# Kernel optimization log

Hardware: AMD Instinct MI355X
Metric: run time of the kernel (lower is better)

## Reference

```python
import jax, jax.numpy as jnp
import numpy as np

B, H, N, D = 2, 16, 2048, 128

def setup_inputs() -> dict:
    key = jax.random.key(0)
    kq, kk, kv = jax.random.split(key, 3)
    q = jax.random.normal(kq, (B, H, N, D), dtype=jnp.float32)
    k = jax.random.normal(kk, (B, H, N, D), dtype=jnp.float32)
    v = jax.random.normal(kv, (B, H, N, D), dtype=jnp.float32)
    return {"q": q, "k": k, "v": v}

def reference(q, k, v):
    # scale = 1/sqrt(d) computed at forward time (scale=None in __init__)
    d = q.shape[-1]
    scale = 1.0 / jnp.sqrt(jnp.asarray(d, dtype=q.dtype))
    # scores: (B, H, N, N)
    scores = jnp.einsum('bhnd,bhmd->bhnm', q, k) * scale
    probs = jax.nn.softmax(scores, axis=-1)
    return jnp.einsum('bhnm,bhmd->bhnd', probs, v)
```

## Files before the change

kernel.cpp:

```cpp
#include <hip/hip_runtime.h>
#include <hip/hip_fp16.h>

#define BH   32
#define SEQ  2048
#define DIM  128
#define CK   32
#define NCH  (SEQ / CK)

typedef _Float16 half8   __attribute__((ext_vector_type(8)));
typedef __fp16   fp16x2  __attribute__((ext_vector_type(2)));
typedef _Float16 half2v  __attribute__((ext_vector_type(2)));
typedef float    floatx4 __attribute__((ext_vector_type(4)));

__device__ inline half2v pk2(float a, float b) {
    fp16x2 t = __builtin_amdgcn_cvt_pkrtz(a, b);
    return *(half2v*)&t;
}
__device__ inline half8 pk8(float4 a, float4 b) {
    half2v l0 = pk2(a.x, a.y), l1 = pk2(a.z, a.w);
    half2v l2 = pk2(b.x, b.y), l3 = pk2(b.z, b.w);
    half8 h;
    h[0] = l0[0]; h[1] = l0[1]; h[2] = l1[0]; h[3] = l1[1];
    h[4] = l2[0]; h[5] = l2[1]; h[6] = l3[0]; h[7] = l3[1];
    return h;
}

__device__ inline void ld16(const void* g, void* l) {
    __builtin_amdgcn_global_load_lds(
        (__attribute__((address_space(1))) void*)(uintptr_t)g,
        (__attribute__((address_space(3))) void*)(uintptr_t)l, 16, 0, 0);
}

#define SYNC_VM8 do {                                          \
    asm volatile("s_waitcnt vmcnt(8)" ::: "memory");           \
    __builtin_amdgcn_s_barrier();                              \
    asm volatile("" ::: "memory");                             \
} while (0)

__global__ void prep_kernel(const float* __restrict__ k, const float* __restrict__ v,
                            _Float16* __restrict__ kh, _Float16* __restrict__ vt) {
    const float SC = 0.08838834764831845f * 1.4426950408889634f;
    __shared__ __align__(16) _Float16 t[32][136];
    const int bh = blockIdx.x >> 6;
    const int kc = blockIdx.x & 63;
    const int tid = threadIdx.x;
    const size_t base = ((size_t)bh * SEQ + kc * CK) * DIM;

    const float4* kf4 = (const float4*)(k + base);
    const float4* vf4 = (const float4*)(v + base);
    half8* kh8 = (half8*)(kh + base);

    #pragma unroll
    for (int i = 0; i < 2; i++) {
        int f8 = i * 256 + tid;
        float4 a = kf4[2 * f8], b = kf4[2 * f8 + 1];
        a.x *= SC; a.y *= SC; a.z *= SC; a.w *= SC;
        b.x *= SC; b.y *= SC; b.z *= SC; b.w *= SC;
        kh8[f8] = pk8(a, b);
        int row = f8 >> 4, c8 = f8 & 15;
        *((half8*)&t[row][c8 * 8]) = pk8(vf4[2 * f8], vf4[2 * f8 + 1]);
    }
    __syncthreads();
    _Float16* vout = vt + ((size_t)bh * NCH + kc) * (DIM * CK);
    #pragma unroll
    for (int i = 0; i < 2; i++) {
        int g = i * 256 + tid;
        int d = g >> 2, kg = g & 3;
        half8 h;
        #pragma unroll
        for (int j = 0; j < 8; j++) h[j] = t[kg * 8 + j][d];
        *((half8*)(vout + d * CK + kg * 8)) = h;
    }
}

__global__ __launch_bounds__(256, 2) void attn_kernel(
        const float* __restrict__ q, const _Float16* __restrict__ kh,
        const _Float16* __restrict__ vt, float* __restrict__ out) {
    __shared__ __align__(16) _Float16 Kbuf[2][CK * DIM];

    const int lid = blockIdx.x + (blockIdx.y << 4);
    const int xcd = lid & 7;
    const int idx = lid >> 3;
    const int bh  = (xcd << 2) + (idx >> 4);
    const int qt  = idx & 15;

    const int tid  = threadIdx.x;
    const int w    = tid >> 6;
    const int lane = tid & 63;
    const int l15  = lane & 15;
    const int quad = lane >> 4;

    half8 qf[2][4];
    #pragma unroll
    for (int s = 0; s < 2; s++) {
        const float* qb = q + ((size_t)bh * SEQ + qt * 128 + w * 32 + s * 16 + l15) * DIM;
        #pragma unroll
        for (int c = 0; c < 4; c++) {
            float4 a = *((const float4*)(qb + c * 32 + quad * 8));
            float4 b = *((const float4*)(qb + c * 32 + quad * 8 + 4));
            qf[s][c] = pk8(a, b);
        }
    }

    half8 ones;
    #pragma unroll
    for (int j = 0; j < 8; j++) ones[j] = (_Float16)1.0f;

    floatx4 zf = {0.f, 0.f, 0.f, 0.f};
    floatx4 O[2][8];
    #pragma unroll
    for (int s = 0; s < 2; s++)
        #pragma unroll
        for (int i = 0; i < 8; i++) O[s][i] = zf;
    floatx4 Osum[2] = {zf, zf};

    const _Float16* kb = kh + (size_t)bh * SEQ * DIM;
    const _Float16* vb = vt + (size_t)bh * SEQ * DIM;

    const int s0 = w * 128 + lane;
    const int s1 = s0 + 64;
    const int rho0 = s0 >> 4, Pos0 = s0 & 15;
    const int rho1 = s1 >> 4, Pos1 = s1 & 15;
    const int g0 = (Pos0 - 3 * rho0) & 15;
    const int g1 = (Pos1 - 3 * rho1) & 15;
    const int key0 = (((rho0 >> 2) & 3) << 3) + ((rho0 >> 4) << 2) + (rho0 & 3);
    const int key1 = (((rho1 >> 2) & 3) << 3) + ((rho1 >> 4) << 2) + (rho1 & 3);
    const _Float16* kgp0 = kb + key0 * DIM + g0 * 8;
    const _Float16* kgp1 = kb + key1 * DIM + g1 * 8;

    auto dma = [&](int kc, int bk_) {
        size_t off = (size_t)kc * (CK * DIM);
        ld16(kgp0 + off, &Kbuf[bk_][(w * 2 + 0) * 512]);
        ld16(kgp1 + off, &Kbuf[bk_][(w * 2 + 1) * 512]);
    };

    const _Float16* vlp = vb + l15 * CK + quad * 8;
    half8 vfr[8];
    auto vload = [&](int kc) {
        const _Float16* p = vlp + (size_t)kc * (CK * DIM);
        #pragma unroll
        for (int dt = 0; dt < 8; dt++)
            vfr[dt] = *((const half8*)(p + dt * 512));
    };

    half8 pf0, pf1;
    #pragma unroll
    for (int j = 0; j < 8; j++) { pf0[j] = (_Float16)0.0f; pf1[j] = (_Float16)0.0f; }

    dma(0, 0);
    vload(0);

    #pragma unroll 2
    for (int kc = 0; kc < NCH; kc++) {
        SYNC_VM8;
        if (kc + 1 < NCH) dma(kc + 1, (kc + 1) & 1);

        const _Float16* Kc = Kbuf[kc & 1];

        floatx4 S[2][2];
        #pragma unroll
        for (int s = 0; s < 2; s++) { S[s][0] = zf; S[s][1] = zf; }
        __builtin_amdgcn_s_setprio(1);
        #pragma unroll
        for (int c = 0; c < 4; c++) {
            #pragma unroll
            for (int j = 0; j < 2; j++) {
                int rho = j * 16 + l15;
                int Pos = (c * 4 + quad + 3 * rho) & 15;
                half8 ka = *((const half8*)&Kc[rho * DIM + Pos * 8]);
                S[0][j] = __builtin_amdgcn_mfma_f32_16x16x32_f16(ka, qf[0][c], S[0][j], 0, 0, 0);
                S[1][j] = __builtin_amdgcn_mfma_f32_16x16x32_f16(ka, qf[1][c], S[1][j], 0, 0, 0);
            }
        }
        __builtin_amdgcn_s_setprio(0);

        half8 pn0, pn1;
        {
            float4 a, b;
            a.x = __builtin_amdgcn_exp2f(S[0][0][0]);
            a.y = __builtin_amdgcn_exp2f(S[0][0][1]);
            a.z = __builtin_amdgcn_exp2f(S[0][0][2]);
            a.w = __builtin_amdgcn_exp2f(S[0][0][3]);
            b.x = __builtin_amdgcn_exp2f(S[0][1][0]);
            b.y = __builtin_amdgcn_exp2f(S[0][1][1]);
            b.z = __builtin_amdgcn_exp2f(S[0][1][2]);
            b.w = __builtin_amdgcn_exp2f(S[0][1][3]);
            pn0 = pk8(a, b);
            a.x = __builtin_amdgcn_exp2f(S[1][0][0]);
            a.y = __builtin_amdgcn_exp2f(S[1][0][1]);
            a.z = __builtin_amdgcn_exp2f(S[1][0][2]);
            a.w = __builtin_amdgcn_exp2f(S[1][0][3]);
            b.x = __builtin_amdgcn_exp2f(S[1][1][0]);
            b.y = __builtin_amdgcn_exp2f(S[1][1][1]);
            b.z = __builtin_amdgcn_exp2f(S[1][1][2]);
            b.w = __builtin_amdgcn_exp2f(S[1][1][3]);
            pn1 = pk8(a, b);
        }

        __builtin_amdgcn_s_setprio(1);
        Osum[0] = __builtin_amdgcn_mfma_f32_16x16x32_f16(pf0, ones, Osum[0], 0, 0, 0);
        Osum[1] = __builtin_amdgcn_mfma_f32_16x16x32_f16(pf1, ones, Osum[1], 0, 0, 0);
        #pragma unroll
        for (int dt = 0; dt < 8; dt++) {
            O[0][dt] = __builtin_amdgcn_mfma_f32_16x16x32_f16(pf0, vfr[dt], O[0][dt], 0, 0, 0);
            O[1][dt] = __builtin_amdgcn_mfma_f32_16x16x32_f16(pf1, vfr[dt], O[1][dt], 0, 0, 0);
        }
        __builtin_amdgcn_s_setprio(0);

        vload(kc);

        pf0 = pn0; pf1 = pn1;
    }

    {
        __builtin_amdgcn_s_setprio(1);
        Osum[0] = __builtin_amdgcn_mfma_f32_16x16x32_f16(pf0, ones, Osum[0], 0, 0, 0);
        Osum[1] = __builtin_amdgcn_mfma_f32_16x16x32_f16(pf1, ones, Osum[1], 0, 0, 0);
        #pragma unroll
        for (int dt = 0; dt < 8; dt++) {
            O[0][dt] = __builtin_amdgcn_mfma_f32_16x16x32_f16(pf0, vfr[dt], O[0][dt], 0, 0, 0);
            O[1][dt] = __builtin_amdgcn_mfma_f32_16x16x32_f16(pf1, vfr[dt], O[1][dt], 0, 0, 0);
        }
        __builtin_amdgcn_s_setprio(0);
    }

    #pragma unroll
    for (int s = 0; s < 2; s++) {
        float* ob = out + ((size_t)bh * SEQ + qt * 128 + w * 32 + s * 16) * DIM;
        #pragma unroll
        for (int r = 0; r < 4; r++) {
            float rinv = 1.0f / Osum[s][r];
            #pragma unroll
            for (int dt = 0; dt < 8; dt++) {
                ob[(size_t)(quad * 4 + r) * DIM + dt * 16 + l15] = O[s][dt][r] * rinv;
            }
        }
    }
}

extern "C" void kernel_launch(void* const* d_in, const int* in_sizes, int n_in,
                              void* d_out, int out_size, void* d_ws, size_t ws_size,
                              hipStream_t stream) {
    const float* q = (const float*)d_in[0];
    const float* k = (const float*)d_in[1];
    const float* v = (const float*)d_in[2];
    float* out = (float*)d_out;

    const size_t elems = (size_t)BH * SEQ * DIM;
    _Float16* kh = (_Float16*)d_ws;
    _Float16* vtp = kh + elems;

    prep_kernel<<<BH * NCH, 256, 0, stream>>>(k, v, kh, vtp);
    attn_kernel<<<dim3(SEQ / 128, BH), 256, 0, stream>>>(q, kh, vtp, out);
}
```

Measured before the change: 207.5 us.

## Split key range across two warp groups and stage V through LDS

Doubles the block to 512 threads. Two groups of four waves each process half of the key chunks for the same 128 query rows, and their partial O and row sums are merged through shared memory at the end. V tiles are now DMA'd into a triple-buffered LDS region alongside K instead of being loaded from global memory into registers, and the wait changes to vmcnt(0). This raises parallelism per query tile and shortens the serial key loop. In exchange it uses more LDS and adds a reduction step, and the launch-bounds change may limit registers.

```diff
diff --git a/kernel.cpp b/kernel.cpp
--- a/kernel.cpp
+++ b/kernel.cpp
@@ -6,6 +6,8 @@
 #define DIM  128
 #define CK   32
 #define NCH  (SEQ / CK)
+#define NSTEP (NCH / 2)
+#define CSZ  (CK * DIM)
 
 typedef _Float16 half8   __attribute__((ext_vector_type(8)));
 typedef __fp16   fp16x2  __attribute__((ext_vector_type(2)));
@@ -31,8 +33,8 @@
         (__attribute__((address_space(3))) void*)(uintptr_t)l, 16, 0, 0);
 }
 
-#define SYNC_VM8 do {                                          \
-    asm volatile("s_waitcnt vmcnt(8)" ::: "memory");           \
+#define SYNC_VM0 do {                                          \
+    asm volatile("s_waitcnt vmcnt(0)" ::: "memory");           \
     __builtin_amdgcn_s_barrier();                              \
     asm volatile("" ::: "memory");                             \
 } while (0)
@@ -73,10 +75,10 @@
     }
 }
 
-__global__ __launch_bounds__(256, 2) void attn_kernel(
+__global__ __launch_bounds__(512, 4) void attn_kernel(
         const float* __restrict__ q, const _Float16* __restrict__ kh,
         const _Float16* __restrict__ vt, float* __restrict__ out) {
-    __shared__ __align__(16) _Float16 Kbuf[2][CK * DIM];
+    __shared__ __align__(16) _Float16 smem[10 * CSZ];
 
     const int lid = blockIdx.x + (blockIdx.y << 4);
     const int xcd = lid & 7;
@@ -85,10 +87,14 @@
     const int qt  = idx & 15;
 
     const int tid  = threadIdx.x;
-    const int w    = tid >> 6;
+    const int g    = tid >> 8;
+    const int w    = (tid >> 6) & 3;
     const int lane = tid & 63;
     const int l15  = lane & 15;
     const int quad = lane >> 4;
+
+    _Float16* Kg = smem + g * (5 * CSZ);
+    _Float16* Vg = Kg + 2 * CSZ;
 
     half8 qf[2][4];
     #pragma unroll
@@ -127,35 +133,33 @@
     const int key1 = (((rho1 >> 2) & 3) << 3) + ((rho1 >> 4) << 2) + (rho1 & 3);
     const _Float16* kgp0 = kb + key0 * DIM + g0 * 8;
     const _Float16* kgp1 = kb + key1 * DIM + g1 * 8;
-
-    auto dma = [&](int kc, int bk_) {
-        size_t off = (size_t)kc * (CK * DIM);
-        ld16(kgp0 + off, &Kbuf[bk_][(w * 2 + 0) * 512]);
-        ld16(kgp1 + off, &Kbuf[bk_][(w * 2 + 1) * 512]);
+    const int vo0 = ((s0 >> 6) * 16 + (s0 & 15)) * CK + ((s0 >> 4) & 3) * 8;
+    const int vo1 = ((s1 >> 6) * 16 + (s1 & 15)) * CK + ((s1 >> 4) & 3) * 8;
+    const _Float16* vgp0 = vb + vo0;
+    const _Float16* vgp1 = vb + vo1;
+
+    const int kcb = g << 5;
+
+    auto dma = [&](int st, int bk_, int bv_) {
+        size_t off = (size_t)(kcb + st) * CSZ;
+        ld16(kgp0 + off, &Kg[bk_ * CSZ + (w * 2 + 0) * 512]);
+        ld16(kgp1 + off, &Kg[bk_ * CSZ + (w * 2 + 1) * 512]);
+        ld16(vgp0 + off, &Vg[bv_ * CSZ + (w * 2 + 0) * 512]);
+        ld16(vgp1 + off, &Vg[bv_ * CSZ + (w * 2 + 1) * 512]);
     };
 
-    const _Float16* vlp = vb + l15 * CK + quad * 8;
+    half8 pf0, pf1;
     half8 vfr[8];
-    auto vload = [&](int kc) {
-        const _Float16* p = vlp + (size_t)kc * (CK * DIM);
-        #pragma unroll
-        for (int dt = 0; dt < 8; dt++)
-            vfr[dt] = *((const half8*)(p + dt * 512));
-    };
-
-    half8 pf0, pf1;
     #pragma unroll
     for (int j = 0; j < 8; j++) { pf0[j] = (_Float16)0.0f; pf1[j] = (_Float16)0.0f; }
-
-    dma(0, 0);
-    vload(0);
-
-    #pragma unroll 2
-    for (int kc = 0; kc < NCH; kc++) {
-        SYNC_VM8;
-        if (kc + 1 < NCH) dma(kc + 1, (kc + 1) & 1);
-
-        const _Float16* Kc = Kbuf[kc & 1];
+    #pragma unroll
+    for (int dt = 0; dt < 8; dt++)
+        #pragma unroll
+        for (int j = 0; j < 8; j++) vfr[dt][j] = (_Float16)0.0f;
+
+    auto body = [&](int bk_, int bvr_) {
+        const _Float16* Kc = Kg + bk_ * CSZ;
+        const _Float16* Vc = Vg + bvr_ * CSZ;
 
         floatx4 S[2][2];
         #pragma unroll
@@ -173,6 +177,11 @@
             }
         }
         __builtin_amdgcn_s_setprio(0);
+
+        half8 vn[8];
+        #pragma unroll
+        for (int dt = 0; dt < 8; dt++)
+            vn[dt] = *((const half8*)&Vc[dt * 512 + (quad * 16 + l15) * 8]);
 
         half8 pn0, pn1;
         {
@@ -207,32 +216,63 @@
         }
         __builtin_amdgcn_s_setprio(0);
 
-        vload(kc);
-
+        #pragma unroll
+        for (int dt = 0; dt < 8; dt++) vfr[dt] = vn[dt];
         pf0 = pn0; pf1 = pn1;
-    }
-
-    {
-        __builtin_amdgcn_s_setprio(1);
-        Osum[0] = __builtin_amdgcn_mfma_f32_16x16x32_f16(pf0, ones, Osum[0], 0, 0, 0);
-        Osum[1] = __builtin_amdgcn_mfma_f32_16x16x32_f16(pf1, ones, Osum[1], 0, 0, 0);
-        #pragma unroll
-        for (int dt = 0; dt < 8; dt++) {
-            O[0][dt] = __builtin_amdgcn_mfma_f32_16x16x32_f16(pf0, vfr[dt], O[0][dt], 0, 0, 0);
-            O[1][dt] = __builtin_amdgcn_mfma_f32_16x16x32_f16(pf1, vfr[dt], O[1][dt], 0, 0, 0);
-        }
-        __builtin_amdgcn_s_setprio(0);
-    }
-
-    #pragma unroll
-    for (int s = 0; s < 2; s++) {
-        float* ob = out + ((size_t)bh * SEQ + qt * 128 + w * 32 + s * 16) * DIM;
-        #pragma unroll
-        for (int r = 0; r < 4; r++) {
-            float rinv = 1.0f / Osum[s][r];
+    };
+
+    dma(0, 0, 0);
+
+    int bvr = 0, bvn = 1;
+    #pragma unroll 2
+    for (int st = 0; st < NSTEP; st++) {
+        SYNC_VM0;
+        if (st + 1 < NSTEP) dma(st + 1, (st + 1) & 1, bvn);
+        body(st & 1, bvr);
+        bvr++; if (bvr == 3) bvr = 0;
+        bvn++; if (bvn == 3) bvn = 0;
+    }
+
+    __builtin_amdgcn_s_setprio(1);
+    Osum[0] = __builtin_amdgcn_mfma_f32_16x16x32_f16(pf0, ones, Osum[0], 0, 0, 0);
+    Osum[1] = __builtin_amdgcn_mfma_f32_16x16x32_f16(pf1, ones, Osum[1], 0, 0, 0);
+    #pragma unroll
+    for (int dt = 0; dt < 8; dt++) {
+        O[0][dt] = __builtin_amdgcn_mfma_f32_16x16x32_f16(pf0, vfr[dt], O[0][dt], 0, 0, 0);
+        O[1][dt] = __builtin_amdgcn_mfma_f32_16x16x32_f16(pf1, vfr[dt], O[1][dt], 0, 0, 0);
+    }
+    __builtin_amdgcn_s_setprio(0);
+
+    const int LDP = 132;
+    float* Old = (float*)smem;
+    float* Sld = ((float*)smem) + DIM * LDP;
+    __syncthreads();
+    if (g == 1) {
+        #pragma unroll
+        for (int s = 0; s < 2; s++)
             #pragma unroll
-            for (int dt = 0; dt < 8; dt++) {
-                ob[(size_t)(quad * 4 + r) * DIM + dt * 16 + l15] = O[s][dt][r] * rinv;
+            for (int r = 0; r < 4; r++) {
+                int row = w * 32 + s * 16 + quad * 4 + r;
+                #pragma unroll
+                for (int dt = 0; dt < 8; dt++)
+                    Old[row * LDP + dt * 16 + l15] = O[s][dt][r];
+                if (l15 == 0) Sld[row] = Osum[s][r];
+            }
+    }
+    __syncthreads();
+    if (g == 0) {
+        #pragma unroll
+        for (int s = 0; s < 2; s++) {
+            float* ob = out + ((size_t)bh * SEQ + qt * 128 + w * 32 + s * 16) * DIM;
+            #pragma unroll
+            for (int r = 0; r < 4; r++) {
+                int row = w * 32 + s * 16 + quad * 4 + r;
+                float rinv = 1.0f / (Osum[s][r] + Sld[row]);
+                #pragma unroll
+                for (int dt = 0; dt < 8; dt++) {
+                    ob[(size_t)(quad * 4 + r) * DIM + dt * 16 + l15] =
+                        (O[s][dt][r] + Old[row * LDP + dt * 16 + l15]) * rinv;
+                }
             }
         }
     }
@@ -251,5 +291,5 @@
     _Float16* vtp = kh + elems;
 
     prep_kernel<<<BH * NCH, 256, 0, stream>>>(k, v, kh, vtp);
-    attn_kernel<<<dim3(SEQ / 128, BH), 256, 0, stream>>>(q, kh, vtp, out);
-}
+    attn_kernel<<<dim3(SEQ / 128, BH), 512, 0, stream>>>(q, kh, vtp, out);
+}
```

Result: slower. 684.7 us (+229.9%).

## Stage V through LDS via async DMA and halve workgroup size to 64 query rows

Applied to the files above, without the earlier changes.

V chunks are now copied into double-buffered LDS with global_load_lds alongside K, and each iteration reads them back from LDS instead of issuing per-lane global register loads. Workgroups shrink to 2 waves covering 64 query rows, with twice as many blocks and an adjusted XCD mapping. The goal is to move V loads onto the asynchronous DMA path and raise occupancy. The trade-off is a full vmcnt(0)/lgkmcnt(0) wait each iteration, which serialises the prefetch more. Each block also reloads K and V for half as many queries, which doubles K/V traffic per query.

```diff
diff --git a/kernel.cpp b/kernel.cpp
--- a/kernel.cpp
+++ b/kernel.cpp
@@ -6,6 +6,7 @@
 #define DIM  128
 #define CK   32
 #define NCH  (SEQ / CK)
+#define CSZ  (CK * DIM)
 
 typedef _Float16 half8   __attribute__((ext_vector_type(8)));
 typedef __fp16   fp16x2  __attribute__((ext_vector_type(2)));
@@ -31,10 +32,10 @@
         (__attribute__((address_space(3))) void*)(uintptr_t)l, 16, 0, 0);
 }
 
-#define SYNC_VM8 do {                                          \
-    asm volatile("s_waitcnt vmcnt(8)" ::: "memory");           \
-    __builtin_amdgcn_s_barrier();                              \
-    asm volatile("" ::: "memory");                             \
+#define SYNC_VML do {                                              \
+    asm volatile("s_waitcnt vmcnt(0) lgkmcnt(0)" ::: "memory");    \
+    __builtin_amdgcn_s_barrier();                                  \
+    asm volatile("" ::: "memory");                                 \
 } while (0)
 
 __global__ void prep_kernel(const float* __restrict__ k, const float* __restrict__ v,
@@ -73,16 +74,17 @@
     }
 }
 
-__global__ __launch_bounds__(256, 2) void attn_kernel(
+__global__ __launch_bounds__(128, 2) void attn_kernel(
         const float* __restrict__ q, const _Float16* __restrict__ kh,
         const _Float16* __restrict__ vt, float* __restrict__ out) {
-    __shared__ __align__(16) _Float16 Kbuf[2][CK * DIM];
-
-    const int lid = blockIdx.x + (blockIdx.y << 4);
+    __shared__ __align__(16) _Float16 Kbuf[2][CSZ];
+    __shared__ __align__(16) _Float16 Vbuf[2][CSZ];
+
+    const int lid = blockIdx.x + (blockIdx.y << 5);
     const int xcd = lid & 7;
     const int idx = lid >> 3;
-    const int bh  = (xcd << 2) + (idx >> 4);
-    const int qt  = idx & 15;
+    const int bh  = (xcd << 2) + (idx >> 5);
+    const int qt  = idx & 31;
 
     const int tid  = threadIdx.x;
     const int w    = tid >> 6;
@@ -93,7 +95,7 @@
     half8 qf[2][4];
     #pragma unroll
     for (int s = 0; s < 2; s++) {
-        const float* qb = q + ((size_t)bh * SEQ + qt * 128 + w * 32 + s * 16 + l15) * DIM;
+        const float* qb = q + ((size_t)bh * SEQ + qt * 64 + w * 32 + s * 16 + l15) * DIM;
         #pragma unroll
         for (int c = 0; c < 4; c++) {
             float4 a = *((const float4*)(qb + c * 32 + quad * 8));
@@ -117,45 +119,40 @@
     const _Float16* kb = kh + (size_t)bh * SEQ * DIM;
     const _Float16* vb = vt + (size_t)bh * SEQ * DIM;
 
-    const int s0 = w * 128 + lane;
-    const int s1 = s0 + 64;
-    const int rho0 = s0 >> 4, Pos0 = s0 & 15;
-    const int rho1 = s1 >> 4, Pos1 = s1 & 15;
-    const int g0 = (Pos0 - 3 * rho0) & 15;
-    const int g1 = (Pos1 - 3 * rho1) & 15;
-    const int key0 = (((rho0 >> 2) & 3) << 3) + ((rho0 >> 4) << 2) + (rho0 & 3);
-    const int key1 = (((rho1 >> 2) & 3) << 3) + ((rho1 >> 4) << 2) + (rho1 & 3);
-    const _Float16* kgp0 = kb + key0 * DIM + g0 * 8;
-    const _Float16* kgp1 = kb + key1 * DIM + g1 * 8;
-
-    auto dma = [&](int kc, int bk_) {
-        size_t off = (size_t)kc * (CK * DIM);
-        ld16(kgp0 + off, &Kbuf[bk_][(w * 2 + 0) * 512]);
-        ld16(kgp1 + off, &Kbuf[bk_][(w * 2 + 1) * 512]);
+    const _Float16* kgp[4];
+    const _Float16* vgp[4];
+    #pragma unroll
+    for (int i = 0; i < 4; i++) {
+        int si = w * 256 + i * 64 + lane;
+        int rho = si >> 4, Pos = si & 15;
+        int g = (Pos - 3 * rho) & 15;
+        int key = (((rho >> 2) & 3) << 3) + ((rho >> 4) << 2) + (rho & 3);
+        kgp[i] = kb + key * DIM + g * 8;
+        int vo = ((si >> 6) * 16 + (si & 15)) * CK + ((si >> 4) & 3) * 8;
+        vgp[i] = vb + vo;
+    }
+
+    auto dma = [&](int kc, int b_) {
+        size_t off = (size_t)kc * CSZ;
+        #pragma unroll
+        for (int i = 0; i < 4; i++) {
+            ld16(kgp[i] + off, &Kbuf[b_][(w * 4 + i) * 512]);
+            ld16(vgp[i] + off, &Vbuf[b_][(w * 4 + i) * 512]);
+        }
     };
 
-    const _Float16* vlp = vb + l15 * CK + quad * 8;
+    half8 pf0, pf1;
     half8 vfr[8];
-    auto vload = [&](int kc) {
-        const _Float16* p = vlp + (size_t)kc * (CK * DIM);
-        #pragma unroll
-        for (int dt = 0; dt < 8; dt++)
-            vfr[dt] = *((const half8*)(p + dt * 512));
-    };
-
-    half8 pf0, pf1;
     #pragma unroll
     for (int j = 0; j < 8; j++) { pf0[j] = (_Float16)0.0f; pf1[j] = (_Float16)0.0f; }
-
-    dma(0, 0);
-    vload(0);
-
-    #pragma unroll 2
-    for (int kc = 0; kc < NCH; kc++) {
-        SYNC_VM8;
-        if (kc + 1 < NCH) dma(kc + 1, (kc + 1) & 1);
-
-        const _Float16* Kc = Kbuf[kc & 1];
+    #pragma unroll
+    for (int dt = 0; dt < 8; dt++)
+        #pragma unroll
+        for (int j = 0; j < 8; j++) vfr[dt][j] = (_Float16)0.0f;
+
+    auto body = [&](int b_) {
+        const _Float16* Kc = Kbuf[b_];
+        const _Float16* Vc = Vbuf[b_];
 
         floatx4 S[2][2];
         #pragma unroll
@@ -173,6 +170,11 @@
             }
         }
         __builtin_amdgcn_s_setprio(0);
+
+        half8 vn[8];
+        #pragma unroll
+        for (int dt = 0; dt < 8; dt++)
+            vn[dt] = *((const half8*)&Vc[dt * 512 + (quad * 16 + l15) * 8]);
 
         half8 pn0, pn1;
         {
@@ -207,26 +209,33 @@
         }
         __builtin_amdgcn_s_setprio(0);
 
-        vload(kc);
-
+        #pragma unroll
+        for (int dt = 0; dt < 8; dt++) vfr[dt] = vn[dt];
         pf0 = pn0; pf1 = pn1;
-    }
-
-    {
-        __builtin_amdgcn_s_setprio(1);
-        Osum[0] = __builtin_amdgcn_mfma_f32_16x16x32_f16(pf0, ones, Osum[0], 0, 0, 0);
-        Osum[1] = __builtin_amdgcn_mfma_f32_16x16x32_f16(pf1, ones, Osum[1], 0, 0, 0);
-        #pragma unroll
-        for (int dt = 0; dt < 8; dt++) {
-            O[0][dt] = __builtin_amdgcn_mfma_f32_16x16x32_f16(pf0, vfr[dt], O[0][dt], 0, 0, 0);
-            O[1][dt] = __builtin_amdgcn_mfma_f32_16x16x32_f16(pf1, vfr[dt], O[1][dt], 0, 0, 0);
-        }
-        __builtin_amdgcn_s_setprio(0);
-    }
+    };
+
+    dma(0, 0);
+
+    #pragma unroll 2
+    for (int kc = 0; kc < NCH; kc++) {
+        SYNC_VML;
+        if (kc + 1 < NCH) dma(kc + 1, (kc + 1) & 1);
+        body(kc & 1);
+    }
+
+    __builtin_amdgcn_s_setprio(1);
+    Osum[0] = __builtin_amdgcn_mfma_f32_16x16x32_f16(pf0, ones, Osum[0], 0, 0, 0);
+    Osum[1] = __builtin_amdgcn_mfma_f32_16x16x32_f16(pf1, ones, Osum[1], 0, 0, 0);
+    #pragma unroll
+    for (int dt = 0; dt < 8; dt++) {
+        O[0][dt] = __builtin_amdgcn_mfma_f32_16x16x32_f16(pf0, vfr[dt], O[0][dt], 0, 0, 0);
+        O[1][dt] = __builtin_amdgcn_mfma_f32_16x16x32_f16(pf1, vfr[dt], O[1][dt], 0, 0, 0);
+    }
+    __builtin_amdgcn_s_setprio(0);
 
     #pragma unroll
     for (int s = 0; s < 2; s++) {
-        float* ob = out + ((size_t)bh * SEQ + qt * 128 + w * 32 + s * 16) * DIM;
+        float* ob = out + ((size_t)bh * SEQ + qt * 64 + w * 32 + s * 16) * DIM;
         #pragma unroll
         for (int r = 0; r < 4; r++) {
             float rinv = 1.0f / Osum[s][r];
@@ -251,5 +260,5 @@
     _Float16* vtp = kh + elems;
 
     prep_kernel<<<BH * NCH, 256, 0, stream>>>(k, v, kh, vtp);
-    attn_kernel<<<dim3(SEQ / 128, BH), 256, 0, stream>>>(q, kh, vtp, out);
-}
+    attn_kernel<<<dim3(SEQ / 64, BH), 128, 0, stream>>>(q, kh, vtp, out);
+}
```

New measurement: 201.8 us. -2.8%, faster.
